# Performance work log

Measured on AMD Instinct MI355X. Metric: run time of the kernel, lower is better.

## Reference

```python
import jax, jax.numpy as jnp
import numpy as np

NUM_TIMES = 1024  # times are drawn from [0, 1024), used as fixed segment count
N = 16777216


def setup_inputs() -> dict:
    key = jax.random.key(0)
    k1, k2, k3 = jax.random.split(key, 3)
    outs = jax.random.normal(k1, (N,), dtype=jnp.float32)
    T_E = jax.random.randint(k2, (N,), 0, 2, dtype=jnp.int32)
    T_T = jax.random.randint(k3, (N,), 0, NUM_TIMES, dtype=jnp.int32)
    return {"outs": outs, "T_E": T_E, "T_T": T_T}


def reference(outs, T_E, T_T):
    # E[E > 0] = 1  -> binary event indicator
    E = (T_E > 0).astype(outs.dtype)
    # Y_label_T = |T_T| ; integer times act directly as segment ids
    seg_ids = jnp.abs(T_T)
    Obs = jnp.sum(E)
    # log of running sum of hazards: log(cumsum(exp(yhat)))
    y_hat_cumsum = jnp.log(jnp.cumsum(jnp.exp(outs)))
    # original segment_max initializes accumulator at 0, so it is clipped below at 0;
    # jnp.maximum also neutralizes -inf fill for empty segments (count=0 there anyway)
    seg_max = jnp.maximum(
        jax.ops.segment_max(y_hat_cumsum, seg_ids, num_segments=NUM_TIMES), 0.0
    )
    seg_cnt = jax.ops.segment_sum(E, seg_ids, num_segments=NUM_TIMES)
    loss_s2 = jnp.sum(seg_max * seg_cnt)
    loss_s1 = jnp.sum(outs * E)
    return (loss_s2 - loss_s1) / Obs
```

## Files before the change

kernel.cpp:

```cpp
#include <hip/hip_runtime.h>

#define NUM_SEGS 1024
#define CHUNK_LOG 13
#define CHUNK (1 << CHUNK_LOG)
#define SUBCH 4
#define SUPER (CHUNK * SUBCH)
#define BLK 256

__device__ __forceinline__ float waveReduceSumF(float v) {
#pragma unroll
    for (int off = 32; off > 0; off >>= 1) v += __shfl_down(v, off, 64);
    return v;
}
__device__ __forceinline__ unsigned waveReduceSumU(unsigned v) {
#pragma unroll
    for (int off = 32; off > 0; off >>= 1) v += __shfl_down(v, off, 64);
    return v;
}

__global__ void init_kernel(unsigned* __restrict__ seg_cnt,
                            int* __restrict__ last_idx,
                            unsigned* __restrict__ obs,
                            double* __restrict__ loss1,
                            double* __restrict__ loss2) {
    int t = blockIdx.x * blockDim.x + threadIdx.x;
    if (t < NUM_SEGS) { seg_cnt[t] = 0u; last_idx[t] = -1; }
    if (t == 0) { obs[0] = 0u; loss1[0] = 0.0; loss2[0] = 0.0; }
}

__global__ __launch_bounds__(BLK) void pass1_kernel(
    const float* __restrict__ outs, const int* __restrict__ te,
    const int* __restrict__ tt, int N, int nChunks,
    float* __restrict__ chunk_sums, unsigned* __restrict__ seg_cnt,
    int* __restrict__ last_idx, unsigned* __restrict__ obs,
    double* __restrict__ loss1) {
    __shared__ unsigned hist[NUM_SEGS];
    __shared__ int lmax[NUM_SEGS];
    __shared__ float redF[BLK / 64];
    __shared__ unsigned redU[BLK / 64];

    for (int t = threadIdx.x; t < NUM_SEGS; t += BLK) { hist[t] = 0u; lmax[t] = -1; }
    __syncthreads();

    float sumOE = 0.f;
    unsigned cntE = 0u;
    const int superBase = blockIdx.x * SUPER;
    const int lane = threadIdx.x & 63;
    const int wid = threadIdx.x >> 6;

#pragma unroll 1
    for (int k = 0; k < SUBCH; ++k) {
        const int cbase = superBase + k * CHUNK;
        float sumExp = 0.f;
        if (cbase + CHUNK <= N) {
#pragma unroll
            for (int it = 0; it < CHUNK / (BLK * 4); ++it) {
                const int i = cbase + it * (BLK * 4) + (threadIdx.x << 2);
                const float4 o = *reinterpret_cast<const float4*>(outs + i);
                const int4 ev = *reinterpret_cast<const int4*>(te + i);
                const int4 sv = *reinterpret_cast<const int4*>(tt + i);
                const float e0 = __expf(o.x), e1 = __expf(o.y);
                const float e2 = __expf(o.z), e3 = __expf(o.w);
                sumExp += (e0 + e1) + (e2 + e3);
                const int s0 = sv.x < 0 ? -sv.x : sv.x;
                const int s1 = sv.y < 0 ? -sv.y : sv.y;
                const int s2 = sv.z < 0 ? -sv.z : sv.z;
                const int s3 = sv.w < 0 ? -sv.w : sv.w;
                atomicMax(&lmax[s0], i);
                atomicMax(&lmax[s1], i + 1);
                atomicMax(&lmax[s2], i + 2);
                atomicMax(&lmax[s3], i + 3);
                if (ev.x > 0) { cntE++; sumOE += o.x; atomicAdd(&hist[s0], 1u); }
                if (ev.y > 0) { cntE++; sumOE += o.y; atomicAdd(&hist[s1], 1u); }
                if (ev.z > 0) { cntE++; sumOE += o.z; atomicAdd(&hist[s2], 1u); }
                if (ev.w > 0) { cntE++; sumOE += o.w; atomicAdd(&hist[s3], 1u); }
            }
        } else {
            const int end = (cbase + CHUNK < N) ? cbase + CHUNK : N;
            for (int i = cbase + (int)threadIdx.x; i < end; i += BLK) {
                const float o = outs[i];
                const int e = te[i];
                int s = tt[i]; s = s < 0 ? -s : s;
                sumExp += __expf(o);
                atomicMax(&lmax[s], i);
                if (e > 0) { cntE++; sumOE += o; atomicAdd(&hist[s], 1u); }
            }
        }
        const float w = waveReduceSumF(sumExp);
        if (lane == 0) redF[wid] = w;
        __syncthreads();
        if (threadIdx.x == 0) {
            const float s4 = (redF[0] + redF[1]) + (redF[2] + redF[3]);
            const int cidx = cbase >> CHUNK_LOG;
            if (cidx < nChunks) chunk_sums[cidx] = s4;
        }
        __syncthreads();
    }

    for (int t = threadIdx.x; t < NUM_SEGS; t += BLK) {
        const unsigned h = hist[t];
        if (h) atomicAdd(&seg_cnt[t], h);
        const int m = lmax[t];
        if (m >= 0) atomicMax(&last_idx[t], m);
    }

    const float wOE = waveReduceSumF(sumOE);
    const unsigned wC = waveReduceSumU(cntE);
    if (lane == 0) { redF[wid] = wOE; redU[wid] = wC; }
    __syncthreads();
    if (threadIdx.x == 0) {
        const float oe = (redF[0] + redF[1]) + (redF[2] + redF[3]);
        const unsigned c = redU[0] + redU[1] + redU[2] + redU[3];
        atomicAdd(loss1, (double)oe);
        atomicAdd(obs, c);
    }
}

__global__ void scan_kernel(const float* __restrict__ csums,
                            double* __restrict__ cprefix, int nChunks) {
    __shared__ double tsum[256];
    const int per = (nChunks + 255) / 256;
    const int start = threadIdx.x * per;
    double s = 0.0;
    for (int j = 0; j < per; ++j) {
        const int c = start + j;
        if (c < nChunks) s += (double)csums[c];
    }
    tsum[threadIdx.x] = s;
    __syncthreads();
    if (threadIdx.x == 0) {
        double acc = 0.0;
        for (int i = 0; i < 256; ++i) { const double t = tsum[i]; tsum[i] = acc; acc += t; }
    }
    __syncthreads();
    double acc = tsum[threadIdx.x];
    for (int j = 0; j < per; ++j) {
        const int c = start + j;
        if (c < nChunks) { cprefix[c] = acc; acc += (double)csums[c]; }
    }
}

__global__ __launch_bounds__(256) void seg_kernel(
    const float* __restrict__ outs, const int* __restrict__ last_idx,
    const unsigned* __restrict__ seg_cnt, const double* __restrict__ cprefix,
    double* __restrict__ loss2) {
    __shared__ float redF[4];
    const int t = blockIdx.x;
    const int li = last_idx[t];
    if (li < 0) return;
    const int c = li >> CHUNK_LOG;
    const int base = c << CHUNK_LOG;
    float s = 0.f;
    for (int i = base + (int)threadIdx.x; i <= li; i += 256) s += __expf(outs[i]);
    const float w = waveReduceSumF(s);
    const int lane = threadIdx.x & 63, wid = threadIdx.x >> 6;
    if (lane == 0) redF[wid] = w;
    __syncthreads();
    if (threadIdx.x == 0) {
        const double S = cprefix[c] + (double)((redF[0] + redF[1]) + (redF[2] + redF[3]));
        double sm = log(S);
        if (sm < 0.0) sm = 0.0;
        atomicAdd(loss2, sm * (double)seg_cnt[t]);
    }
}

__global__ void final_kernel(const double* __restrict__ loss1,
                             const double* __restrict__ loss2,
                             const unsigned* __restrict__ obs,
                             float* __restrict__ out) {
    out[0] = (float)((loss2[0] - loss1[0]) / (double)obs[0]);
}

extern "C" void kernel_launch(void* const* d_in, const int* in_sizes, int n_in,
                              void* d_out, int out_size, void* d_ws, size_t ws_size,
                              hipStream_t stream) {
    const float* outs = (const float*)d_in[0];
    const int* te = (const int*)d_in[1];
    const int* tt = (const int*)d_in[2];
    const int N = in_sizes[0];
    float* out = (float*)d_out;

    const int nChunks = (N + CHUNK - 1) / CHUNK;

    char* ws = (char*)d_ws;
    double* d_loss1 = (double*)ws;
    double* d_loss2 = d_loss1 + 1;
    double* d_cprefix = (double*)(ws + 16);
    float* d_csums = (float*)(d_cprefix + nChunks);
    int* d_lastidx = (int*)(d_csums + nChunks);
    unsigned* d_segcnt = (unsigned*)(d_lastidx + NUM_SEGS);
    unsigned* d_obs = d_segcnt + NUM_SEGS;

    init_kernel<<<(NUM_SEGS + 255) / 256, 256, 0, stream>>>(d_segcnt, d_lastidx,
                                                            d_obs, d_loss1, d_loss2);
    const int nSuper = (N + SUPER - 1) / SUPER;
    pass1_kernel<<<nSuper, BLK, 0, stream>>>(outs, te, tt, N, nChunks, d_csums,
                                             d_segcnt, d_lastidx, d_obs, d_loss1);
    scan_kernel<<<1, 256, 0, stream>>>(d_csums, d_cprefix, nChunks);
    seg_kernel<<<NUM_SEGS, 256, 0, stream>>>(outs, d_lastidx, d_segcnt, d_cprefix,
                                             d_loss2);
    final_kernel<<<1, 1, 0, stream>>>(d_loss1, d_loss2, d_obs, out);
}
```

Before: 232.9 us.

## Use one block per chunk, drop scan and final kernels, prefetch loads

pass1 now launches one block per 8K-element chunk instead of one per four chunks, so there are four times as many blocks; each block also software-prefetches the next vector loads. The separate scan kernel is removed: each seg block sums the preceding chunk sums itself in double and vectorizes its tail exp-sum. The final kernel is folded into seg_kernel through a last-block-done atomic counter. This cuts two launches and raises memory parallelism in the main pass, at the cost of four times as many per-block histogram flushes to global atomics and redundant prefix sums in every seg block.

```diff
diff --git a/kernel.cpp b/kernel.cpp
--- a/kernel.cpp
+++ b/kernel.cpp
@@ -3,9 +3,8 @@
 #define NUM_SEGS 1024
 #define CHUNK_LOG 13
 #define CHUNK (1 << CHUNK_LOG)
-#define SUBCH 4
-#define SUPER (CHUNK * SUBCH)
 #define BLK 256
+#define ITERS (CHUNK / (BLK * 4))
 
 __device__ __forceinline__ float waveReduceSumF(float v) {
 #pragma unroll
@@ -17,85 +16,86 @@
     for (int off = 32; off > 0; off >>= 1) v += __shfl_down(v, off, 64);
     return v;
 }
+__device__ __forceinline__ double waveReduceSumD(double v) {
+#pragma unroll
+    for (int off = 32; off > 0; off >>= 1) v += __shfl_down(v, off, 64);
+    return v;
+}
 
 __global__ void init_kernel(unsigned* __restrict__ seg_cnt,
                             int* __restrict__ last_idx,
                             unsigned* __restrict__ obs,
                             double* __restrict__ loss1,
-                            double* __restrict__ loss2) {
+                            double* __restrict__ loss2,
+                            unsigned* __restrict__ counter) {
     int t = blockIdx.x * blockDim.x + threadIdx.x;
     if (t < NUM_SEGS) { seg_cnt[t] = 0u; last_idx[t] = -1; }
-    if (t == 0) { obs[0] = 0u; loss1[0] = 0.0; loss2[0] = 0.0; }
+    if (t == 0) { obs[0] = 0u; loss1[0] = 0.0; loss2[0] = 0.0; counter[0] = 0u; }
 }
 
 __global__ __launch_bounds__(BLK) void pass1_kernel(
     const float* __restrict__ outs, const int* __restrict__ te,
-    const int* __restrict__ tt, int N, int nChunks,
+    const int* __restrict__ tt, int N,
     float* __restrict__ chunk_sums, unsigned* __restrict__ seg_cnt,
     int* __restrict__ last_idx, unsigned* __restrict__ obs,
     double* __restrict__ loss1) {
     __shared__ unsigned hist[NUM_SEGS];
     __shared__ int lmax[NUM_SEGS];
-    __shared__ float redF[BLK / 64];
+    __shared__ float redE[BLK / 64];
+    __shared__ float redOE[BLK / 64];
     __shared__ unsigned redU[BLK / 64];
 
     for (int t = threadIdx.x; t < NUM_SEGS; t += BLK) { hist[t] = 0u; lmax[t] = -1; }
     __syncthreads();
 
-    float sumOE = 0.f;
+    float sumExp = 0.f, sumOE = 0.f;
     unsigned cntE = 0u;
-    const int superBase = blockIdx.x * SUPER;
-    const int lane = threadIdx.x & 63;
-    const int wid = threadIdx.x >> 6;
+    const int cbase = blockIdx.x * CHUNK;
 
-#pragma unroll 1
-    for (int k = 0; k < SUBCH; ++k) {
-        const int cbase = superBase + k * CHUNK;
-        float sumExp = 0.f;
-        if (cbase + CHUNK <= N) {
+    if (cbase + CHUNK <= N) {
+        const float4* o4 = reinterpret_cast<const float4*>(outs);
+        const int4* e4 = reinterpret_cast<const int4*>(te);
+        const int4* s4 = reinterpret_cast<const int4*>(tt);
+        const int vbase = (cbase >> 2) + (int)threadIdx.x;
+        float4 o = o4[vbase];
+        int4 ev = e4[vbase];
+        int4 sv = s4[vbase];
 #pragma unroll
-            for (int it = 0; it < CHUNK / (BLK * 4); ++it) {
-                const int i = cbase + it * (BLK * 4) + (threadIdx.x << 2);
-                const float4 o = *reinterpret_cast<const float4*>(outs + i);
-                const int4 ev = *reinterpret_cast<const int4*>(te + i);
-                const int4 sv = *reinterpret_cast<const int4*>(tt + i);
-                const float e0 = __expf(o.x), e1 = __expf(o.y);
-                const float e2 = __expf(o.z), e3 = __expf(o.w);
-                sumExp += (e0 + e1) + (e2 + e3);
-                const int s0 = sv.x < 0 ? -sv.x : sv.x;
-                const int s1 = sv.y < 0 ? -sv.y : sv.y;
-                const int s2 = sv.z < 0 ? -sv.z : sv.z;
-                const int s3 = sv.w < 0 ? -sv.w : sv.w;
-                atomicMax(&lmax[s0], i);
-                atomicMax(&lmax[s1], i + 1);
-                atomicMax(&lmax[s2], i + 2);
-                atomicMax(&lmax[s3], i + 3);
-                if (ev.x > 0) { cntE++; sumOE += o.x; atomicAdd(&hist[s0], 1u); }
-                if (ev.y > 0) { cntE++; sumOE += o.y; atomicAdd(&hist[s1], 1u); }
-                if (ev.z > 0) { cntE++; sumOE += o.z; atomicAdd(&hist[s2], 1u); }
-                if (ev.w > 0) { cntE++; sumOE += o.w; atomicAdd(&hist[s3], 1u); }
+        for (int it = 0; it < ITERS; ++it) {
+            const float4 oc = o;
+            const int4 evc = ev;
+            const int4 svc = sv;
+            if (it + 1 < ITERS) {
+                const int v2 = vbase + (it + 1) * BLK;
+                o = o4[v2]; ev = e4[v2]; sv = s4[v2];
             }
-        } else {
-            const int end = (cbase + CHUNK < N) ? cbase + CHUNK : N;
-            for (int i = cbase + (int)threadIdx.x; i < end; i += BLK) {
-                const float o = outs[i];
-                const int e = te[i];
-                int s = tt[i]; s = s < 0 ? -s : s;
-                sumExp += __expf(o);
-                atomicMax(&lmax[s], i);
-                if (e > 0) { cntE++; sumOE += o; atomicAdd(&hist[s], 1u); }
-            }
+            const int i = (vbase + it * BLK) << 2;
+            const int s0 = svc.x < 0 ? -svc.x : svc.x;
+            const int s1 = svc.y < 0 ? -svc.y : svc.y;
+            const int s2 = svc.z < 0 ? -svc.z : svc.z;
+            const int s3 = svc.w < 0 ? -svc.w : svc.w;
+            atomicMax(&lmax[s0], i);
+            atomicMax(&lmax[s1], i + 1);
+            atomicMax(&lmax[s2], i + 2);
+            atomicMax(&lmax[s3], i + 3);
+            sumExp += (__expf(oc.x) + __expf(oc.y)) + (__expf(oc.z) + __expf(oc.w));
+            if (evc.x > 0) { cntE++; sumOE += oc.x; atomicAdd(&hist[s0], 1u); }
+            if (evc.y > 0) { cntE++; sumOE += oc.y; atomicAdd(&hist[s1], 1u); }
+            if (evc.z > 0) { cntE++; sumOE += oc.z; atomicAdd(&hist[s2], 1u); }
+            if (evc.w > 0) { cntE++; sumOE += oc.w; atomicAdd(&hist[s3], 1u); }
         }
-        const float w = waveReduceSumF(sumExp);
-        if (lane == 0) redF[wid] = w;
-        __syncthreads();
-        if (threadIdx.x == 0) {
-            const float s4 = (redF[0] + redF[1]) + (redF[2] + redF[3]);
-            const int cidx = cbase >> CHUNK_LOG;
-            if (cidx < nChunks) chunk_sums[cidx] = s4;
+    } else {
+        const int end = N;
+        for (int i = cbase + (int)threadIdx.x; i < end; i += BLK) {
+            const float o = outs[i];
+            const int e = te[i];
+            int s = tt[i]; s = s < 0 ? -s : s;
+            sumExp += __expf(o);
+            atomicMax(&lmax[s], i);
+            if (e > 0) { cntE++; sumOE += o; atomicAdd(&hist[s], 1u); }
         }
-        __syncthreads();
     }
+    __syncthreads();
 
     for (int t = threadIdx.x; t < NUM_SEGS; t += BLK) {
         const unsigned h = hist[t];
@@ -104,71 +104,66 @@
         if (m >= 0) atomicMax(&last_idx[t], m);
     }
 
+    const float wE = waveReduceSumF(sumExp);
     const float wOE = waveReduceSumF(sumOE);
     const unsigned wC = waveReduceSumU(cntE);
-    if (lane == 0) { redF[wid] = wOE; redU[wid] = wC; }
+    const int lane = threadIdx.x & 63, wid = threadIdx.x >> 6;
+    if (lane == 0) { redE[wid] = wE; redOE[wid] = wOE; redU[wid] = wC; }
     __syncthreads();
     if (threadIdx.x == 0) {
-        const float oe = (redF[0] + redF[1]) + (redF[2] + redF[3]);
-        const unsigned c = redU[0] + redU[1] + redU[2] + redU[3];
-        atomicAdd(loss1, (double)oe);
-        atomicAdd(obs, c);
-    }
-}
-
-__global__ void scan_kernel(const float* __restrict__ csums,
-                            double* __restrict__ cprefix, int nChunks) {
-    __shared__ double tsum[256];
-    const int per = (nChunks + 255) / 256;
-    const int start = threadIdx.x * per;
-    double s = 0.0;
-    for (int j = 0; j < per; ++j) {
-        const int c = start + j;
-        if (c < nChunks) s += (double)csums[c];
-    }
-    tsum[threadIdx.x] = s;
-    __syncthreads();
-    if (threadIdx.x == 0) {
-        double acc = 0.0;
-        for (int i = 0; i < 256; ++i) { const double t = tsum[i]; tsum[i] = acc; acc += t; }
-    }
-    __syncthreads();
-    double acc = tsum[threadIdx.x];
-    for (int j = 0; j < per; ++j) {
-        const int c = start + j;
-        if (c < nChunks) { cprefix[c] = acc; acc += (double)csums[c]; }
+        chunk_sums[blockIdx.x] = (redE[0] + redE[1]) + (redE[2] + redE[3]);
+        atomicAdd(loss1, (double)((redOE[0] + redOE[1]) + (redOE[2] + redOE[3])));
+        atomicAdd(obs, redU[0] + redU[1] + redU[2] + redU[3]);
     }
 }
 
 __global__ __launch_bounds__(256) void seg_kernel(
-    const float* __restrict__ outs, const int* __restrict__ last_idx,
-    const unsigned* __restrict__ seg_cnt, const double* __restrict__ cprefix,
-    double* __restrict__ loss2) {
-    __shared__ float redF[4];
+    const float* __restrict__ outs, const float* __restrict__ csums,
+    const int* __restrict__ last_idx, const unsigned* __restrict__ seg_cnt,
+    const double* __restrict__ loss1, double* __restrict__ loss2,
+    const unsigned* __restrict__ obs, unsigned* __restrict__ counter,
+    float* __restrict__ out) {
+    __shared__ double redD[4];
     const int t = blockIdx.x;
     const int li = last_idx[t];
-    if (li < 0) return;
-    const int c = li >> CHUNK_LOG;
-    const int base = c << CHUNK_LOG;
-    float s = 0.f;
-    for (int i = base + (int)threadIdx.x; i <= li; i += 256) s += __expf(outs[i]);
-    const float w = waveReduceSumF(s);
-    const int lane = threadIdx.x & 63, wid = threadIdx.x >> 6;
-    if (lane == 0) redF[wid] = w;
+    if (li >= 0) {
+        const int c = li >> CHUNK_LOG;
+        double ps = 0.0;
+        for (int j = threadIdx.x; j < c; j += 256) ps += (double)csums[j];
+        const int base = c << CHUNK_LOG;
+        const int n = li - base + 1;
+        const int nv = n >> 2;
+        const float4* p4 = reinterpret_cast<const float4*>(outs + base);
+        float fs = 0.f;
+        for (int j = threadIdx.x; j < nv; j += 256) {
+            const float4 v = p4[j];
+            fs += (__expf(v.x) + __expf(v.y)) + (__expf(v.z) + __expf(v.w));
+        }
+        if ((int)threadIdx.x < (n & 3)) fs += __expf(outs[base + (nv << 2) + (int)threadIdx.x]);
+        ps += (double)fs;
+        const double w = waveReduceSumD(ps);
+        const int lane = threadIdx.x & 63, wid = threadIdx.x >> 6;
+        if (lane == 0) redD[wid] = w;
+        __syncthreads();
+        if (threadIdx.x == 0) {
+            const double S = (redD[0] + redD[1]) + (redD[2] + redD[3]);
+            double sm = log(S);
+            if (sm < 0.0) sm = 0.0;
+            atomicAdd(loss2, sm * (double)seg_cnt[t]);
+        }
+    }
     __syncthreads();
     if (threadIdx.x == 0) {
-        const double S = cprefix[c] + (double)((redF[0] + redF[1]) + (redF[2] + redF[3]));
-        double sm = log(S);
-        if (sm < 0.0) sm = 0.0;
-        atomicAdd(loss2, sm * (double)seg_cnt[t]);
+        __threadfence();
+        const unsigned done = atomicAdd(counter, 1u);
+        if (done == gridDim.x - 1) {
+            __threadfence();
+            const double l2 = atomicAdd(loss2, 0.0);
+            const double l1 = loss1[0];
+            const unsigned ob = obs[0];
+            out[0] = (float)((l2 - l1) / (double)ob);
+        }
     }
-}
-
-__global__ void final_kernel(const double* __restrict__ loss1,
-                             const double* __restrict__ loss2,
-                             const unsigned* __restrict__ obs,
-                             float* __restrict__ out) {
-    out[0] = (float)((loss2[0] - loss1[0]) / (double)obs[0]);
 }
 
 extern "C" void kernel_launch(void* const* d_in, const int* in_sizes, int n_in,
@@ -185,19 +180,16 @@
     char* ws = (char*)d_ws;
     double* d_loss1 = (double*)ws;
     double* d_loss2 = d_loss1 + 1;
-    double* d_cprefix = (double*)(ws + 16);
-    float* d_csums = (float*)(d_cprefix + nChunks);
+    unsigned* d_obs = (unsigned*)(ws + 16);
+    unsigned* d_counter = d_obs + 1;
+    float* d_csums = (float*)(ws + 32);
     int* d_lastidx = (int*)(d_csums + nChunks);
     unsigned* d_segcnt = (unsigned*)(d_lastidx + NUM_SEGS);
-    unsigned* d_obs = d_segcnt + NUM_SEGS;
 
-    init_kernel<<<(NUM_SEGS + 255) / 256, 256, 0, stream>>>(d_segcnt, d_lastidx,
-                                                            d_obs, d_loss1, d_loss2);
-    const int nSuper = (N + SUPER - 1) / SUPER;
-    pass1_kernel<<<nSuper, BLK, 0, stream>>>(outs, te, tt, N, nChunks, d_csums,
-                                             d_segcnt, d_lastidx, d_obs, d_loss1);
-    scan_kernel<<<1, 256, 0, stream>>>(d_csums, d_cprefix, nChunks);
-    seg_kernel<<<NUM_SEGS, 256, 0, stream>>>(outs, d_lastidx, d_segcnt, d_cprefix,
-                                             d_loss2);
-    final_kernel<<<1, 1, 0, stream>>>(d_loss1, d_loss2, d_obs, out);
+    init_kernel<<<(NUM_SEGS + 255) / 256, 256, 0, stream>>>(
+        d_segcnt, d_lastidx, d_obs, d_loss1, d_loss2, d_counter);
+    pass1_kernel<<<nChunks, BLK, 0, stream>>>(outs, te, tt, N, d_csums, d_segcnt,
+                                              d_lastidx, d_obs, d_loss1);
+    seg_kernel<<<NUM_SEGS, 256, 0, stream>>>(outs, d_csums, d_lastidx, d_segcnt,
+                                             d_loss1, d_loss2, d_obs, d_counter, out);
 }
```

Result: slower. 245.7 us (+5.5%).
